# Kernel tuning notes

Measured on AMD Instinct MI355X. Metric: run time of the kernel, lower is better.

## Reference

```python
import jax, jax.numpy as jnp
import numpy as np

N_NODES = 10000
N_EDGES = 320000
N_GRAPHS = 64
IN_DIM = 1
HID = 256


def setup_inputs() -> dict:
    key = jax.random.key(0)
    ks = jax.random.split(key, 12)
    s = 1.0 / np.sqrt(HID)
    inp = {
        "x": jax.random.normal(ks[0], (N_NODES, IN_DIM), dtype=jnp.float32),
        "edge_index": jax.random.randint(ks[1], (2, N_EDGES), 0, N_NODES, dtype=jnp.int64),
        "batch": jnp.sort(jax.random.randint(ks[2], (N_NODES,), 0, N_GRAPHS, dtype=jnp.int64)),
        "W_emb": jax.random.normal(ks[3], (IN_DIM, HID), dtype=jnp.float32),
        "b_emb": jnp.zeros((HID,), dtype=jnp.float32),
        "W1a": jax.random.normal(ks[4], (HID, HID), dtype=jnp.float32) * s,
        "b1a": jnp.zeros((HID,), dtype=jnp.float32),
        "W1b": jax.random.normal(ks[5], (HID, HID), dtype=jnp.float32) * s,
        "b1b": jnp.zeros((HID,), dtype=jnp.float32),
        "W2a": jax.random.normal(ks[6], (HID, HID), dtype=jnp.float32) * s,
        "b2a": jnp.zeros((HID,), dtype=jnp.float32),
        "W2b": jax.random.normal(ks[7], (HID, HID), dtype=jnp.float32) * s,
        "b2b": jnp.zeros((HID,), dtype=jnp.float32),
    }
    return inp


def _pointnet_conv(h, src, dst, Wa, ba, Wb, bb):
    # gather x_j -> 2-layer MLP per edge -> scatter-max at dst (PyG aggr='max')
    msg = jax.nn.relu(h[src] @ Wa + ba) @ Wb + bb          # [E, HID]
    agg = jax.ops.segment_max(msg, dst, num_segments=N_NODES)
    # PyG fills nodes with no incoming messages with 0
    return jnp.where(jnp.isneginf(agg), 0.0, agg)


def reference(x, edge_index, batch, W_emb, b_emb, W1a, b1a, W1b, b1b, W2a, b2a, W2b, b2b):
    src, dst = edge_index[0], edge_index[1]
    h = jax.nn.silu(x @ W_emb + b_emb)                     # [N, HID]
    h = h + jax.nn.silu(_pointnet_conv(h, src, dst, W1a, b1a, W1b, b1b))
    h = h + jax.nn.silu(_pointnet_conv(h, src, dst, W2a, b2a, W2b, b2b))
    # global_mean_pool over graphs
    sums = jax.ops.segment_sum(h, batch, num_segments=N_GRAPHS)          # [G, HID]
    cnts = jax.ops.segment_sum(jnp.ones((h.shape[0],), h.dtype), batch, num_segments=N_GRAPHS)
    return sums / jnp.maximum(cnts, 1.0)[:, None]
```

## Files before the change

### kernel.cpp

```cpp
#include <hip/hip_runtime.h>
#include <hip/hip_bf16.h>
#include <math.h>

#define HID 256
#define CAP 128

typedef __attribute__((ext_vector_type(8))) short bf16x8;
typedef __attribute__((ext_vector_type(4))) float f32x4;

__device__ __forceinline__ float silu_f(float z) {
    return z / (1.0f + __expf(-z));
}
__device__ __forceinline__ unsigned short f2bf(float f) {
    unsigned int u = __float_as_uint(f);
    u = (u + 0x7FFFu + ((u >> 16) & 1u)) >> 16;
    return (unsigned short)u;
}
__device__ __forceinline__ float bf2f(unsigned short b) {
    return __uint_as_float(((unsigned int)b) << 16);
}
__device__ __forceinline__ void max4(float4& m, ushort4 v) {
    m.x = fmaxf(m.x, bf2f(v.x));
    m.y = fmaxf(m.y, bf2f(v.y));
    m.z = fmaxf(m.z, bf2f(v.z));
    m.w = fmaxf(m.w, bf2f(v.w));
}

__global__ __launch_bounds__(256) void k_prep(
    const float* __restrict__ w0, const float* __restrict__ w1,
    const float* __restrict__ w2, const float* __restrict__ w3,
    unsigned short* __restrict__ o0, unsigned short* __restrict__ o1,
    unsigned short* __restrict__ o2, unsigned short* __restrict__ o3,
    const int* __restrict__ src, const int* __restrict__ dst,
    int* __restrict__ cnt, int* __restrict__ csr,
    const int* __restrict__ batch, int* __restrict__ goff,
    int N, int E, int G, int nh) {
    int b = blockIdx.x;
    int tid = threadIdx.x;
    if (b < 1024) {
        int i = b * 256 + tid;
        int which = i >> 16;
        int j = i & 65535;
        int n = j >> 8, k = j & 255;
        const float* in = (which == 0) ? w0 : (which == 1) ? w1 : (which == 2) ? w2 : w3;
        unsigned short* out = (which == 0) ? o0 : (which == 1) ? o1 : (which == 2) ? o2 : o3;
        out[n * HID + k] = f2bf(in[k * HID + n]);
    } else if (b < 1024 + nh) {
        int e = (b - 1024) * 256 + tid;
        if (e < E) {
            int d = dst[e];
            int p = atomicAdd(&cnt[d], 1);
            if (p < CAP) csr[d * CAP + p] = src[e];
        }
    } else {
        int g = tid;
        if (g > G) return;
        int lo = 0, hi = N;
        while (lo < hi) {
            int mid = (lo + hi) >> 1;
            if (batch[mid] < g) lo = mid + 1; else hi = mid;
        }
        goff[g] = lo;
    }
}

template <bool FIRST>
__global__ __launch_bounds__(256) void k_mlp(
    const float* __restrict__ x, const float* __restrict__ Wemb,
    const float* __restrict__ bemb, const unsigned short* __restrict__ Aglob,
    const unsigned short* __restrict__ Wta, const float* __restrict__ ba,
    const unsigned short* __restrict__ Wtb, const float* __restrict__ bbv,
    float* __restrict__ h, unsigned short* __restrict__ t2, int M) {
    __shared__ unsigned short As[32][264];
    __shared__ unsigned short t1s[32][264];
    int tid = threadIdx.x;
    int lane = tid & 63;
    int wave = tid >> 6;
    int quad = lane >> 4;
    int r = lane & 15;
    int m0 = blockIdx.x * 32;
    int colw = wave * 64;

    if (FIRST) {
        int row = tid >> 3;
        int c0 = (tid & 7) * 32;
        int grow = m0 + row;
        float xv = (grow < M) ? x[grow] : 0.0f;
#pragma unroll
        for (int j = 0; j < 8; ++j) {
            int c = c0 + j * 4;
            float4 v;
            v.x = silu_f(xv * Wemb[c + 0] + bemb[c + 0]);
            v.y = silu_f(xv * Wemb[c + 1] + bemb[c + 1]);
            v.z = silu_f(xv * Wemb[c + 2] + bemb[c + 2]);
            v.w = silu_f(xv * Wemb[c + 3] + bemb[c + 3]);
            if (grow < M) *(float4*)(h + (size_t)grow * HID + c) = v;
            ushort4 q;
            q.x = f2bf(v.x); q.y = f2bf(v.y); q.z = f2bf(v.z); q.w = f2bf(v.w);
            *(ushort4*)&As[row][c] = q;
        }
        __syncthreads();
    }

    f32x4 acc[2][4];
#pragma unroll
    for (int rt = 0; rt < 2; ++rt)
#pragma unroll
        for (int nt = 0; nt < 4; ++nt) acc[rt][nt] = (f32x4)0.0f;

    int ar0 = m0 + r;        if (ar0 >= M) ar0 = M - 1;
    int ar1 = m0 + 16 + r;   if (ar1 >= M) ar1 = M - 1;

#pragma unroll
    for (int ks = 0; ks < 8; ++ks) {
        bf16x8 a0, a1;
        if (FIRST) {
            a0 = *(const bf16x8*)&As[r][ks * 32 + quad * 8];
            a1 = *(const bf16x8*)&As[r + 16][ks * 32 + quad * 8];
        } else {
            a0 = *(const bf16x8*)(Aglob + (size_t)ar0 * HID + ks * 32 + quad * 8);
            a1 = *(const bf16x8*)(Aglob + (size_t)ar1 * HID + ks * 32 + quad * 8);
        }
#pragma unroll
        for (int nt = 0; nt < 4; ++nt) {
            bf16x8 bfr = *(const bf16x8*)(Wta + (size_t)(colw + nt * 16 + r) * HID
                                          + ks * 32 + quad * 8);
            acc[0][nt] = __builtin_amdgcn_mfma_f32_16x16x32_bf16(a0, bfr, acc[0][nt], 0, 0, 0);
            acc[1][nt] = __builtin_amdgcn_mfma_f32_16x16x32_bf16(a1, bfr, acc[1][nt], 0, 0, 0);
        }
    }

#pragma unroll
    for (int nt = 0; nt < 4; ++nt) {
        int col = colw + nt * 16 + r;
        float bv = ba[col];
#pragma unroll
        for (int rt = 0; rt < 2; ++rt)
#pragma unroll
            for (int i = 0; i < 4; ++i) {
                float v = fmaxf(acc[rt][i + 0][0 * 4 + 0], 0.0f);
            }
    }
#pragma unroll
    for (int nt = 0; nt < 4; ++nt) {
        int col = colw + nt * 16 + r;
        float bv = ba[col];
#pragma unroll
        for (int rt = 0; rt < 2; ++rt)
#pragma unroll
            for (int i = 0; i < 4; ++i) {
                float v = fmaxf(acc[rt][nt][i] + bv, 0.0f);
                t1s[rt * 16 + quad * 4 + i][col] = f2bf(v);
            }
    }
    __syncthreads();

    f32x4 acc2[2][4];
#pragma unroll
    for (int rt = 0; rt < 2; ++rt)
#pragma unroll
        for (int nt = 0; nt < 4; ++nt) acc2[rt][nt] = (f32x4)0.0f;
#pragma unroll
    for (int ks = 0; ks < 8; ++ks) {
        bf16x8 a0 = *(const bf16x8*)&t1s[r][ks * 32 + quad * 8];
        bf16x8 a1 = *(const bf16x8*)&t1s[r + 16][ks * 32 + quad * 8];
#pragma unroll
        for (int nt = 0; nt < 4; ++nt) {
            bf16x8 bfr = *(const bf16x8*)(Wtb + (size_t)(colw + nt * 16 + r) * HID
                                          + ks * 32 + quad * 8);
            acc2[0][nt] = __builtin_amdgcn_mfma_f32_16x16x32_bf16(a0, bfr, acc2[0][nt], 0, 0, 0);
            acc2[1][nt] = __builtin_amdgcn_mfma_f32_16x16x32_bf16(a1, bfr, acc2[1][nt], 0, 0, 0);
        }
    }

#pragma unroll
    for (int nt = 0; nt < 4; ++nt) {
        int col = colw + nt * 16 + r;
        float bv = bbv[col];
#pragma unroll
        for (int rt = 0; rt < 2; ++rt)
#pragma unroll
            for (int i = 0; i < 4; ++i) {
                int row = m0 + rt * 16 + quad * 4 + i;
                if (row < M) t2[(size_t)row * HID + col] = f2bf(acc2[rt][nt][i] + bv);
            }
    }
}

__global__ __launch_bounds__(256) void k_agg(const unsigned short* __restrict__ t2,
                                             const int* __restrict__ cnt,
                                             const int* __restrict__ csr,
                                             float* __restrict__ h,
                                             unsigned short* __restrict__ hb, int N) {
    __shared__ float4 red[4][64];
    int node = blockIdx.x;
    int wave = threadIdx.x >> 6;
    int lane = threadIdx.x & 63;
    int deg = cnt[node];
    if (deg > CAP) deg = CAP;
    const int* row = csr + (size_t)node * CAP;

    float4 m = make_float4(-INFINITY, -INFINITY, -INFINITY, -INFINITY);
    int per = (deg + 3) >> 2;
    int lo = wave * per;
    int hi = lo + per; if (hi > deg) hi = deg;
    const unsigned short* base = t2 + lane * 4;
    int i = lo;
    int lim = (hi > lo) ? lo + ((hi - lo) & ~3) : lo;
    for (; i < lim; i += 4) {
        int s0 = row[i + 0], s1 = row[i + 1], s2 = row[i + 2], s3 = row[i + 3];
        ushort4 v0 = *(const ushort4*)(base + (size_t)s0 * HID);
        ushort4 v1 = *(const ushort4*)(base + (size_t)s1 * HID);
        ushort4 v2 = *(const ushort4*)(base + (size_t)s2 * HID);
        ushort4 v3 = *(const ushort4*)(base + (size_t)s3 * HID);
        max4(m, v0); max4(m, v1); max4(m, v2); max4(m, v3);
    }
    for (; i < hi; ++i) {
        int s = row[i];
        ushort4 v = *(const ushort4*)(base + (size_t)s * HID);
        max4(m, v);
    }
    red[wave][lane] = m;
    __syncthreads();
    if (wave == 0) {
        float4 m1 = red[1][lane], m2 = red[2][lane], m3 = red[3][lane];
        m.x = fmaxf(fmaxf(m.x, m1.x), fmaxf(m2.x, m3.x));
        m.y = fmaxf(fmaxf(m.y, m1.y), fmaxf(m2.y, m3.y));
        m.z = fmaxf(fmaxf(m.z, m1.z), fmaxf(m2.z, m3.z));
        m.w = fmaxf(fmaxf(m.w, m1.w), fmaxf(m2.w, m3.w));
        if (deg == 0) m = make_float4(0.f, 0.f, 0.f, 0.f);

        size_t o = (size_t)node * HID + lane * 4;
        float4 hv = *(float4*)(h + o);
        hv.x += silu_f(m.x);
        hv.y += silu_f(m.y);
        hv.z += silu_f(m.z);
        hv.w += silu_f(m.w);
        *(float4*)(h + o) = hv;
        ushort4 q;
        q.x = f2bf(hv.x); q.y = f2bf(hv.y); q.z = f2bf(hv.z); q.w = f2bf(hv.w);
        *(ushort4*)(hb + o) = q;
    }
}

__global__ __launch_bounds__(1024) void k_pool(const float* __restrict__ h,
                                               const int* __restrict__ goff,
                                               float* __restrict__ out) {
    __shared__ float part[3][HID];
    int g = blockIdx.x;
    int tid = threadIdx.x;
    int c = tid & 255;
    int chunk = tid >> 8;
    int beg = goff[g], end = goff[g + 1];
    float s = 0.f;
    for (int n = beg + chunk; n < end; n += 4) s += h[(size_t)n * HID + c];
    if (chunk > 0) part[chunk - 1][c] = s;
    __syncthreads();
    if (chunk == 0) {
        s += part[0][c] + part[1][c] + part[2][c];
        int cnt = end - beg;
        out[g * HID + c] = s / (float)(cnt > 0 ? cnt : 1);
    }
}

extern "C" void kernel_launch(void* const* d_in, const int* in_sizes, int n_in,
                              void* d_out, int out_size, void* d_ws, size_t ws_size,
                              hipStream_t stream) {
    const float* x     = (const float*)d_in[0];
    const int*   ei    = (const int*)d_in[1];
    const int*   batch = (const int*)d_in[2];
    const float* Wemb  = (const float*)d_in[3];
    const float* bemb  = (const float*)d_in[4];
    const float* W1a   = (const float*)d_in[5];
    const float* b1a   = (const float*)d_in[6];
    const float* W1b   = (const float*)d_in[7];
    const float* b1b   = (const float*)d_in[8];
    const float* W2a   = (const float*)d_in[9];
    const float* b2a   = (const float*)d_in[10];
    const float* W2b   = (const float*)d_in[11];
    const float* b2b   = (const float*)d_in[12];
    float* out = (float*)d_out;

    const int N = in_sizes[0];
    const int E = in_sizes[1] / 2;
    const int G = out_size / HID;
    const int* src = ei;
    const int* dst = ei + E;

    char* ws = (char*)d_ws;
    float*          h    = (float*)ws;          ws += (size_t)N * HID * 4;
    unsigned short* hb   = (unsigned short*)ws; ws += (size_t)N * HID * 2;
    unsigned short* t2   = (unsigned short*)ws; ws += (size_t)N * HID * 2;
    unsigned short* Wt1a = (unsigned short*)ws; ws += (size_t)HID * HID * 2;
    unsigned short* Wt1b = (unsigned short*)ws; ws += (size_t)HID * HID * 2;
    unsigned short* Wt2a = (unsigned short*)ws; ws += (size_t)HID * HID * 2;
    unsigned short* Wt2b = (unsigned short*)ws; ws += (size_t)HID * HID * 2;
    int* cnt  = (int*)ws; ws += (size_t)N * 4;
    int* goff = (int*)ws; ws += (size_t)(G + 1) * 4;
    int* csr  = (int*)ws; ws += (size_t)N * CAP * 4;

    const int nh = (E + 255) / 256;

    hipMemsetAsync(cnt, 0, (size_t)N * 4, stream);

    k_prep<<<1024 + nh + 1, 256, 0, stream>>>(W1a, W1b, W2a, W2b,
                                              Wt1a, Wt1b, Wt2a, Wt2b,
                                              src, dst, cnt, csr,
                                              batch, goff, N, E, G, nh);

    dim3 mgrid((N + 31) / 32);

    k_mlp<true ><<<mgrid, 256, 0, stream>>>(x, Wemb, bemb, nullptr,
                                            Wt1a, b1a, Wt1b, b1b, h, t2, N);
    k_agg<<<N, 256, 0, stream>>>(t2, cnt, csr, h, hb, N);

    k_mlp<false><<<mgrid, 256, 0, stream>>>(nullptr, nullptr, nullptr, hb,
                                            Wt2a, b2a, Wt2b, b2b, nullptr, t2, N);
    k_agg<<<N, 256, 0, stream>>>(t2, cnt, csr, h, hb, N);

    k_pool<<<G, 1024, 0, stream>>>(h, goff, out);
}
```

Measured before the change: 219.7 us.

## Drop fp32 residual buffer, fuse mean-pool into last aggregation via atomics

Removes the fp32 hidden-state buffer and keeps the residual stream only in bf16, which cuts global read and write traffic in the embedding and aggregation kernels. The final k_pool kernel is removed: the last aggregation multiplies by a precomputed inverse graph count and atomically adds into an output zeroed inside the prep kernel. The gather loop is also unrolled to eight outstanding loads. In exchange, the residual now accumulates in bf16, and the float atomic adds make the sum order nondeterministic and contend on 64 graph rows.

```diff
diff --git a/kernel.cpp b/kernel.cpp
--- a/kernel.cpp
+++ b/kernel.cpp
@@ -33,7 +33,8 @@
     unsigned short* __restrict__ o2, unsigned short* __restrict__ o3,
     const int* __restrict__ src, const int* __restrict__ dst,
     int* __restrict__ cnt, int* __restrict__ csr,
-    const int* __restrict__ batch, int* __restrict__ goff,
+    const int* __restrict__ batch, float* __restrict__ inv_cnt,
+    float* __restrict__ out, int out_elems,
     int N, int E, int G, int nh) {
     int b = blockIdx.x;
     int tid = threadIdx.x;
@@ -43,8 +44,8 @@
         int j = i & 65535;
         int n = j >> 8, k = j & 255;
         const float* in = (which == 0) ? w0 : (which == 1) ? w1 : (which == 2) ? w2 : w3;
-        unsigned short* out = (which == 0) ? o0 : (which == 1) ? o1 : (which == 2) ? o2 : o3;
-        out[n * HID + k] = f2bf(in[k * HID + n]);
+        unsigned short* op = (which == 0) ? o0 : (which == 1) ? o1 : (which == 2) ? o2 : o3;
+        op[n * HID + k] = f2bf(in[k * HID + n]);
     } else if (b < 1024 + nh) {
         int e = (b - 1024) * 256 + tid;
         if (e < E) {
@@ -52,15 +53,24 @@
             int p = atomicAdd(&cnt[d], 1);
             if (p < CAP) csr[d * CAP + p] = src[e];
         }
+    } else if (b == 1024 + nh) {
+        __shared__ int sg[257];
+        if (tid <= G) {
+            int lo = 0, hi = N;
+            while (lo < hi) {
+                int mid = (lo + hi) >> 1;
+                if (batch[mid] < tid) lo = mid + 1; else hi = mid;
+            }
+            sg[tid] = lo;
+        }
+        __syncthreads();
+        if (tid < G) {
+            int c = sg[tid + 1] - sg[tid];
+            inv_cnt[tid] = 1.0f / (float)(c > 0 ? c : 1);
+        }
     } else {
-        int g = tid;
-        if (g > G) return;
-        int lo = 0, hi = N;
-        while (lo < hi) {
-            int mid = (lo + hi) >> 1;
-            if (batch[mid] < g) lo = mid + 1; else hi = mid;
-        }
-        goff[g] = lo;
+        int i = (b - 1024 - nh - 1) * 256 + tid;
+        if (i < out_elems) out[i] = 0.0f;
     }
 }
 
@@ -70,8 +80,8 @@
     const float* __restrict__ bemb, const unsigned short* __restrict__ Aglob,
     const unsigned short* __restrict__ Wta, const float* __restrict__ ba,
     const unsigned short* __restrict__ Wtb, const float* __restrict__ bbv,
-    float* __restrict__ h, unsigned short* __restrict__ t2, int M) {
-    __shared__ unsigned short As[32][264];
+    unsigned short* __restrict__ hb, unsigned short* __restrict__ t2, int M) {
+    __shared__ unsigned short As[FIRST ? 32 : 1][264];
     __shared__ unsigned short t1s[32][264];
     int tid = threadIdx.x;
     int lane = tid & 63;
@@ -89,14 +99,12 @@
 #pragma unroll
         for (int j = 0; j < 8; ++j) {
             int c = c0 + j * 4;
-            float4 v;
-            v.x = silu_f(xv * Wemb[c + 0] + bemb[c + 0]);
-            v.y = silu_f(xv * Wemb[c + 1] + bemb[c + 1]);
-            v.z = silu_f(xv * Wemb[c + 2] + bemb[c + 2]);
-            v.w = silu_f(xv * Wemb[c + 3] + bemb[c + 3]);
-            if (grow < M) *(float4*)(h + (size_t)grow * HID + c) = v;
             ushort4 q;
-            q.x = f2bf(v.x); q.y = f2bf(v.y); q.z = f2bf(v.z); q.w = f2bf(v.w);
+            q.x = f2bf(silu_f(xv * Wemb[c + 0] + bemb[c + 0]));
+            q.y = f2bf(silu_f(xv * Wemb[c + 1] + bemb[c + 1]));
+            q.z = f2bf(silu_f(xv * Wemb[c + 2] + bemb[c + 2]));
+            q.w = f2bf(silu_f(xv * Wemb[c + 3] + bemb[c + 3]));
+            if (grow < M) *(ushort4*)(hb + (size_t)grow * HID + c) = q;
             *(ushort4*)&As[row][c] = q;
         }
         __syncthreads();
@@ -116,7 +124,7 @@
         bf16x8 a0, a1;
         if (FIRST) {
             a0 = *(const bf16x8*)&As[r][ks * 32 + quad * 8];
-            a1 = *(const bf16x8*)&As[r + 16][ks * 32 + quad * 8];
+            a1 = *(const bf16x8*)&As[(FIRST ? r + 16 : 0)][ks * 32 + quad * 8];
         } else {
             a0 = *(const bf16x8*)(Aglob + (size_t)ar0 * HID + ks * 32 + quad * 8);
             a1 = *(const bf16x8*)(Aglob + (size_t)ar1 * HID + ks * 32 + quad * 8);
@@ -138,17 +146,6 @@
         for (int rt = 0; rt < 2; ++rt)
 #pragma unroll
             for (int i = 0; i < 4; ++i) {
-                float v = fmaxf(acc[rt][i + 0][0 * 4 + 0], 0.0f);
-            }
-    }
-#pragma unroll
-    for (int nt = 0; nt < 4; ++nt) {
-        int col = colw + nt * 16 + r;
-        float bv = ba[col];
-#pragma unroll
-        for (int rt = 0; rt < 2; ++rt)
-#pragma unroll
-            for (int i = 0; i < 4; ++i) {
                 float v = fmaxf(acc[rt][nt][i] + bv, 0.0f);
                 t1s[rt * 16 + quad * 4 + i][col] = f2bf(v);
             }
@@ -187,18 +184,21 @@
     }
 }
 
+template <bool LAST>
 __global__ __launch_bounds__(256) void k_agg(const unsigned short* __restrict__ t2,
                                              const int* __restrict__ cnt,
                                              const int* __restrict__ csr,
-                                             float* __restrict__ h,
-                                             unsigned short* __restrict__ hb, int N) {
+                                             unsigned short* __restrict__ hb,
+                                             const int* __restrict__ batch,
+                                             const float* __restrict__ inv_cnt,
+                                             float* __restrict__ out, int N) {
     __shared__ float4 red[4][64];
     int node = blockIdx.x;
     int wave = threadIdx.x >> 6;
     int lane = threadIdx.x & 63;
     int deg = cnt[node];
     if (deg > CAP) deg = CAP;
-    const int* row = csr + (size_t)node * CAP;
+    const int* rowp = csr + (size_t)node * CAP;
 
     float4 m = make_float4(-INFINITY, -INFINITY, -INFINITY, -INFINITY);
     int per = (deg + 3) >> 2;
@@ -206,17 +206,29 @@
     int hi = lo + per; if (hi > deg) hi = deg;
     const unsigned short* base = t2 + lane * 4;
     int i = lo;
-    int lim = (hi > lo) ? lo + ((hi - lo) & ~3) : lo;
-    for (; i < lim; i += 4) {
-        int s0 = row[i + 0], s1 = row[i + 1], s2 = row[i + 2], s3 = row[i + 3];
-        ushort4 v0 = *(const ushort4*)(base + (size_t)s0 * HID);
-        ushort4 v1 = *(const ushort4*)(base + (size_t)s1 * HID);
-        ushort4 v2 = *(const ushort4*)(base + (size_t)s2 * HID);
-        ushort4 v3 = *(const ushort4*)(base + (size_t)s3 * HID);
-        max4(m, v0); max4(m, v1); max4(m, v2); max4(m, v3);
+    for (; i + 8 <= hi; i += 8) {
+        int s[8];
+#pragma unroll
+        for (int j = 0; j < 8; ++j) s[j] = rowp[i + j];
+        ushort4 v[8];
+#pragma unroll
+        for (int j = 0; j < 8; ++j) v[j] = *(const ushort4*)(base + (size_t)s[j] * HID);
+#pragma unroll
+        for (int j = 0; j < 8; ++j) max4(m, v[j]);
+    }
+    if (i + 4 <= hi) {
+        int s[4];
+#pragma unroll
+        for (int j = 0; j < 4; ++j) s[j] = rowp[i + j];
+        ushort4 v[4];
+#pragma unroll
+        for (int j = 0; j < 4; ++j) v[j] = *(const ushort4*)(base + (size_t)s[j] * HID);
+#pragma unroll
+        for (int j = 0; j < 4; ++j) max4(m, v[j]);
+        i += 4;
     }
     for (; i < hi; ++i) {
-        int s = row[i];
+        int s = rowp[i];
         ushort4 v = *(const ushort4*)(base + (size_t)s * HID);
         max4(m, v);
     }
@@ -231,35 +243,25 @@
         if (deg == 0) m = make_float4(0.f, 0.f, 0.f, 0.f);
 
         size_t o = (size_t)node * HID + lane * 4;
-        float4 hv = *(float4*)(h + o);
-        hv.x += silu_f(m.x);
-        hv.y += silu_f(m.y);
-        hv.z += silu_f(m.z);
-        hv.w += silu_f(m.w);
-        *(float4*)(h + o) = hv;
-        ushort4 q;
-        q.x = f2bf(hv.x); q.y = f2bf(hv.y); q.z = f2bf(hv.z); q.w = f2bf(hv.w);
-        *(ushort4*)(hb + o) = q;
-    }
-}
-
-__global__ __launch_bounds__(1024) void k_pool(const float* __restrict__ h,
-                                               const int* __restrict__ goff,
-                                               float* __restrict__ out) {
-    __shared__ float part[3][HID];
-    int g = blockIdx.x;
-    int tid = threadIdx.x;
-    int c = tid & 255;
-    int chunk = tid >> 8;
-    int beg = goff[g], end = goff[g + 1];
-    float s = 0.f;
-    for (int n = beg + chunk; n < end; n += 4) s += h[(size_t)n * HID + c];
-    if (chunk > 0) part[chunk - 1][c] = s;
-    __syncthreads();
-    if (chunk == 0) {
-        s += part[0][c] + part[1][c] + part[2][c];
-        int cnt = end - beg;
-        out[g * HID + c] = s / (float)(cnt > 0 ? cnt : 1);
+        ushort4 hq = *(const ushort4*)(hb + o);
+        float4 hv;
+        hv.x = bf2f(hq.x) + silu_f(m.x);
+        hv.y = bf2f(hq.y) + silu_f(m.y);
+        hv.z = bf2f(hq.z) + silu_f(m.z);
+        hv.w = bf2f(hq.w) + silu_f(m.w);
+        if (LAST) {
+            int g = batch[node];
+            float ic = inv_cnt[g];
+            float* op = out + (size_t)g * HID + lane * 4;
+            atomicAdd(op + 0, hv.x * ic);
+            atomicAdd(op + 1, hv.y * ic);
+            atomicAdd(op + 2, hv.z * ic);
+            atomicAdd(op + 3, hv.w * ic);
+        } else {
+            ushort4 q;
+            q.x = f2bf(hv.x); q.y = f2bf(hv.y); q.z = f2bf(hv.z); q.w = f2bf(hv.w);
+            *(ushort4*)(hb + o) = q;
+        }
     }
 }
 
@@ -288,35 +290,34 @@
     const int* dst = ei + E;
 
     char* ws = (char*)d_ws;
-    float*          h    = (float*)ws;          ws += (size_t)N * HID * 4;
     unsigned short* hb   = (unsigned short*)ws; ws += (size_t)N * HID * 2;
     unsigned short* t2   = (unsigned short*)ws; ws += (size_t)N * HID * 2;
     unsigned short* Wt1a = (unsigned short*)ws; ws += (size_t)HID * HID * 2;
     unsigned short* Wt1b = (unsigned short*)ws; ws += (size_t)HID * HID * 2;
     unsigned short* Wt2a = (unsigned short*)ws; ws += (size_t)HID * HID * 2;
     unsigned short* Wt2b = (unsigned short*)ws; ws += (size_t)HID * HID * 2;
-    int* cnt  = (int*)ws; ws += (size_t)N * 4;
-    int* goff = (int*)ws; ws += (size_t)(G + 1) * 4;
-    int* csr  = (int*)ws; ws += (size_t)N * CAP * 4;
+    int*   cnt     = (int*)ws;   ws += (size_t)N * 4;
+    float* inv_cnt = (float*)ws; ws += (size_t)G * 4;
+    int*   csr     = (int*)ws;   ws += (size_t)N * CAP * 4;
 
     const int nh = (E + 255) / 256;
+    const int nz = (out_size + 255) / 256;
 
     hipMemsetAsync(cnt, 0, (size_t)N * 4, stream);
 
-    k_prep<<<1024 + nh + 1, 256, 0, stream>>>(W1a, W1b, W2a, W2b,
-                                              Wt1a, Wt1b, Wt2a, Wt2b,
-                                              src, dst, cnt, csr,
-                                              batch, goff, N, E, G, nh);
+    k_prep<<<1024 + nh + 1 + nz, 256, 0, stream>>>(W1a, W1b, W2a, W2b,
+                                                   Wt1a, Wt1b, Wt2a, Wt2b,
+                                                   src, dst, cnt, csr,
+                                                   batch, inv_cnt, out, out_size,
+                                                   N, E, G, nh);
 
     dim3 mgrid((N + 31) / 32);
 
     k_mlp<true ><<<mgrid, 256, 0, stream>>>(x, Wemb, bemb, nullptr,
-                                            Wt1a, b1a, Wt1b, b1b, h, t2, N);
-    k_agg<<<N, 256, 0, stream>>>(t2, cnt, csr, h, hb, N);
+                                            Wt1a, b1a, Wt1b, b1b, hb, t2, N);
+    k_agg<false><<<N, 256, 0, stream>>>(t2, cnt, csr, hb, batch, inv_cnt, out, N);
 
     k_mlp<false><<<mgrid, 256, 0, stream>>>(nullptr, nullptr, nullptr, hb,
-                                            Wt2a, b2a, Wt2b, b2b, nullptr, t2, N);
-    k_agg<<<N, 256, 0, stream>>>(t2, cnt, csr, h, hb, N);
-
-    k_pool<<<G, 1024, 0, stream>>>(h, goff, out);
-}
+                                            Wt2a, b2a, Wt2b, b2b, hb, t2, N);
+    k_agg<true ><<<N, 256, 0, stream>>>(t2, cnt, csr, hb, batch, inv_cnt, out, N);
+}
```

Result: slower. 239.7 us (+9.1%).
